# Optimization experiments

Hardware: AMD Instinct MI355X
Metric: run time of the kernel (lower is better)

## Reference

```python
import jax, jax.numpy as jnp
import numpy as np

NUM_CLASSES = 90
MAX_DET_POINTS = 5000
MAX_DET_PER_IMAGE = 100
IOU_THR = 0.5
NEG = -1e10
IMAGE_SIZE = 768


def _make_anchors(image_size=IMAGE_SIZE, min_level=3, num_levels=5, anchor_scale=4.0):
    """EfficientDet-style anchors, ordered (level, y, x, anchor-config), yxyx."""
    boxes_all = []
    for li in range(num_levels):
        stride = 2 ** (min_level + li)
        boxes_level = []
        for octave in range(3):
            for aspect in (1.0, 2.0, 0.5):
                base = anchor_scale * stride * 2.0 ** (octave / 3.0)
                ax = np.sqrt(aspect)
                half_x = base * ax / 2.0
                half_y = base / ax / 2.0
                x = np.arange(stride / 2.0, image_size, stride)
                y = np.arange(stride / 2.0, image_size, stride)
                xv, yv = np.meshgrid(x, y)  # [H, W], row-major matches NHWC flatten
                xv = xv.reshape(-1)
                yv = yv.reshape(-1)
                boxes = np.stack([yv - half_y, xv - half_x, yv + half_y, xv + half_x], axis=1)
                boxes_level.append(boxes[:, None, :])
        boxes_all.append(np.concatenate(boxes_level, axis=1).reshape(-1, 4))
    return np.concatenate(boxes_all, axis=0).astype(np.float32)


def setup_inputs() -> dict:
    key = jax.random.key(0)
    ks = jax.random.split(key, 10)
    B = 8
    hw = [96, 48, 24, 12, 6]
    inp = {}
    for i, s in enumerate(hw):
        inp[f"cls{i}"] = jax.random.normal(ks[i], (B, 810, s, s), jnp.float32)
        inp[f"box{i}"] = jax.random.normal(ks[5 + i], (B, 36, s, s), jnp.float32)
    inp["anchor_boxes"] = jnp.asarray(_make_anchors())
    return inp


def _decode_boxes(rel_codes, anchors):
    # anchors: yxyx; rel_codes: (ty, tx, th, tw) -> output xyxy
    ycenter_a = (anchors[..., 0] + anchors[..., 2]) / 2
    xcenter_a = (anchors[..., 1] + anchors[..., 3]) / 2
    ha = anchors[..., 2] - anchors[..., 0]
    wa = anchors[..., 3] - anchors[..., 1]
    ty, tx, th, tw = rel_codes[..., 0], rel_codes[..., 1], rel_codes[..., 2], rel_codes[..., 3]
    w = jnp.exp(tw) * wa
    h = jnp.exp(th) * ha
    yc = ty * ha + ycenter_a
    xc = tx * wa + xcenter_a
    return jnp.stack([xc - w / 2, yc - h / 2, xc + w / 2, yc + h / 2], axis=-1)


def _nms_indices(boxes, scores, classes, iou_thr=IOU_THR, max_out=MAX_DET_PER_IMAGE):
    """torchvision.batched_nms: class-offset boxes, greedy NMS, return idx + valid mask."""
    boxes = jax.lax.stop_gradient(boxes)
    scores = jax.lax.stop_gradient(scores)
    off = classes.astype(boxes.dtype) * (jnp.max(boxes) + 1.0)
    b = boxes + off[:, None]  # [N,4]
    area = (b[:, 2] - b[:, 0]) * (b[:, 3] - b[:, 1])

    def body(i, state):
        live, sel, val = state
        idx = jnp.argmax(live)
        ok = live[idx] > 0.0  # sigmoid scores are >0; suppressed are NEG
        bi = b[idx]
        ix = jnp.maximum(0.0, jnp.minimum(b[:, 2], bi[2]) - jnp.maximum(b[:, 0], bi[0]))
        iy = jnp.maximum(0.0, jnp.minimum(b[:, 3], bi[3]) - jnp.maximum(b[:, 1], bi[1]))
        inter = ix * iy
        iou = inter / (area + area[idx] - inter + 1e-8)
        live = jnp.where(iou > iou_thr, NEG, live).at[idx].set(NEG)
        return live, sel.at[i].set(idx), val.at[i].set(ok)

    state0 = (scores, jnp.zeros((max_out,), jnp.int32), jnp.zeros((max_out,), bool))
    _, sel, val = jax.lax.fori_loop(0, max_out, body, state0)
    return sel, val


def _forward(cls_levels, box_levels, anchor_boxes):
    B = cls_levels[0].shape[0]
    C = NUM_CLASSES
    # NCHW -> NHWC -> [B, A, C] / [B, A, 4], concat over levels
    cls_all = jnp.concatenate(
        [c.transpose(0, 2, 3, 1).reshape(B, -1, C) for c in cls_levels], axis=1)
    box_all = jnp.concatenate(
        [b.transpose(0, 2, 3, 1).reshape(B, -1, 4) for b in box_levels], axis=1)

    top_vals, top_idx = jax.lax.top_k(cls_all.reshape(B, -1), MAX_DET_POINTS)
    indices = top_idx // C  # anchor index
    classes = top_idx % C
    box_topk = jnp.take_along_axis(box_all, indices[..., None], axis=1)  # [B,K,4]
    anchors_sel = anchor_boxes[indices]  # [B,K,4]

    boxes = _decode_boxes(box_topk, anchors_sel)  # xyxy [B,K,4]
    scores = jax.nn.sigmoid(top_vals)  # [B,K]

    def per_image(bx, sc, cl):
        sel, val = _nms_indices(bx, sc, cl)
        det = jnp.concatenate(
            [bx[sel], sc[sel, None], (cl[sel] + 1).astype(bx.dtype)[:, None]], axis=1)
        return jnp.where(val[:, None], det, 0.0)  # pad invalid rows with zeros

    return jax.vmap(per_image)(boxes, scores, classes)  # [B, 100, 6]


def reference(cls0, cls1, cls2, cls3, cls4, box0, box1, box2, box3, box4, anchor_boxes):
    return _forward((cls0, cls1, cls2, cls3, cls4), (box0, box1, box2, box3, box4), anchor_boxes)
```

## Files before the change

kernel.cpp:

```cpp
#include <hip/hip_runtime.h>
#include <stdint.h>

#define KDET 5000
#define MAX_OUT 100
#define PRE_THR 2.5f
#define CAND_CAP 98304u
#define SEL_N 8192u
#define TOTAL_F 9943560u
#define STAGE_CAP 1024u
#define HBINS 2048u
#define FB 0x18040u
#define SEL_STRIDE 5120u

#define WS_CNT   0
#define WS_HIST  4096
#define WS_PMAX  69632
#define WS_CAND  131072
#define WS_SELG  6422528
#define WS_BX    6750208
#define WS_SC    7390208
#define WS_CL    7550208

__device__ __forceinline__ unsigned f2key(float f) {
  unsigned u = __float_as_uint(f);
  return u ^ (unsigned)(((int)u >> 31) | 0x80000000);
}

__global__ __launch_bounds__(256, 8) void scan_kernel(
    const float* __restrict__ c0, const float* __restrict__ c1,
    const float* __restrict__ c2, const float* __restrict__ c3,
    const float* __restrict__ c4,
    unsigned long long* __restrict__ cand,
    unsigned* __restrict__ cnt, unsigned* __restrict__ hist)
{
  __shared__ unsigned sh_hist[HBINS];
  __shared__ unsigned long long sh_cand[STAGE_CAP];
  __shared__ unsigned sh_ccnt;
  __shared__ unsigned sh_base;

  const unsigned img = blockIdx.y;
  const unsigned tid = threadIdx.x;
  const float* ptrs[5] = {c0, c1, c2, c3, c4};
  const unsigned lvlElems[5] = {7464960u, 1866240u, 466560u, 116640u, 29160u};
  const unsigned hw2s[5] = {9216u, 2304u, 576u, 144u, 36u};
  const unsigned fbases[5] = {0u, 7464960u, 9331200u, 9797760u, 9914400u};
  unsigned long long* candI = cand + (size_t)img * CAND_CAP;
  unsigned* histI = hist + img * HBINS;

  for (unsigned b = tid; b < HBINS; b += 256u) sh_hist[b] = 0u;
  if (tid == 0) sh_ccnt = 0u;
  __syncthreads();

#pragma unroll
  for (int lev = 0; lev < 5; ++lev) {
    const float4* p = (const float4*)(ptrs[lev] + (size_t)img * lvlElems[lev]);
    const unsigned n4 = lvlElems[lev] >> 2;
    const unsigned hw2 = hw2s[lev];
    const unsigned fbase = fbases[lev];
    const unsigned chunk = 256u * 4u;
    const unsigned sweep = gridDim.x * chunk;
    for (unsigned s0 = blockIdx.x * chunk; s0 < n4; s0 += sweep) {
      float4 v[4]; unsigned idxs[4]; bool ok[4];
#pragma unroll
      for (int u = 0; u < 4; ++u) {
        idxs[u] = s0 + (unsigned)u * 256u + tid;
        ok[u] = idxs[u] < n4;
        if (ok[u]) v[u] = p[idxs[u]];
      }
#pragma unroll
      for (int u = 0; u < 4; ++u) {
        if (!ok[u]) continue;
        float vs[4] = {v[u].x, v[u].y, v[u].z, v[u].w};
#pragma unroll
        for (int j = 0; j < 4; ++j) {
          float f = vs[j];
          if (f > PRE_THR) {
            unsigned key = f2key(f);
            unsigned bin = (key >> 15) - FB;
            if (bin > HBINS - 1u) bin = HBINS - 1u;
            atomicAdd(&sh_hist[bin], 1u);
            unsigned linear = idxs[u] * 4u + (unsigned)j;
            unsigned ch = linear / hw2;
            unsigned pos = linear - ch * hw2;
            unsigned F = fbase + pos * 810u + ch;
            unsigned slot = atomicAdd(&sh_ccnt, 1u);
            if (slot < STAGE_CAP)
              sh_cand[slot] = ((unsigned long long)key << 32) | (unsigned)(~F);
          }
        }
      }
    }
  }
  __syncthreads();

  unsigned n = sh_ccnt < STAGE_CAP ? sh_ccnt : STAGE_CAP;
  if (tid == 0) sh_base = atomicAdd(&cnt[img], n);
  __syncthreads();
  unsigned base = sh_base;
  for (unsigned k = tid; k < n; k += 256u) {
    unsigned slot = base + k;
    if (slot < CAND_CAP) candI[slot] = sh_cand[k];
  }
  for (unsigned b = tid; b < HBINS; b += 256u) {
    unsigned v = sh_hist[b];
    if (v) atomicAdd(&histI[b], v);
  }
}

__device__ __forceinline__ void bitonic_ce(unsigned long long* sb,
                                           unsigned i, unsigned ixj, bool desc) {
  unsigned long long a = sb[i], b = sb[ixj];
  if ((a < b) == desc) { sb[i] = b; sb[ixj] = a; }
}

__global__ __launch_bounds__(1024) void sort_kernel(
    const unsigned long long* __restrict__ cand, const unsigned* __restrict__ cnt,
    const unsigned* __restrict__ hist, unsigned long long* __restrict__ selG)
{
  const unsigned img = blockIdx.x;
  const unsigned tid = threadIdx.x;
  const unsigned wid = tid >> 6, lane = tid & 63u;
  __shared__ unsigned long long sb[SEL_N];
  __shared__ unsigned wsum[16];
  __shared__ unsigned sh_keyLow;
  __shared__ unsigned sh_scnt;

  const unsigned* histI = hist + img * HBINS;
  unsigned b0 = 2047u - 2u * tid;
  unsigned b1 = b0 - 1u;
  unsigned h0 = histI[b0], h1 = histI[b1];
  unsigned s = h0 + h1;
  unsigned inc = s;
#pragma unroll
  for (int off = 1; off < 64; off <<= 1) {
    unsigned nv = __shfl_up(inc, off, 64);
    if ((int)lane >= off) inc += nv;
  }
  if (lane == 63u) wsum[wid] = inc;
  if (tid == 0) { sh_keyLow = 0u; sh_scnt = 0u; }
  __syncthreads();
  if (tid < 64u) {
    unsigned v = (tid < 16u) ? wsum[tid] : 0u;
#pragma unroll
    for (int off = 1; off < 16; off <<= 1) {
      unsigned nv = __shfl_up(v, off, 64);
      if ((int)tid >= off) v += nv;
    }
    if (tid < 16u) wsum[tid] = v;
  }
  __syncthreads();
  unsigned excl = inc - s + (wid ? wsum[wid - 1] : 0u);
  if (excl < (unsigned)KDET && excl + s >= (unsigned)KDET) {
    unsigned binr = (excl + h0 >= (unsigned)KDET) ? b0 : b1;
    sh_keyLow = (binr + FB) << 15;
  }
  __syncthreads();
  const unsigned keyLow = sh_keyLow;

  unsigned M = cnt[img]; if (M > CAND_CAP) M = CAND_CAP;
  const unsigned long long* candI = cand + (size_t)img * CAND_CAP;
  for (unsigned i = tid; i < M; i += 1024u) {
    unsigned long long c = candI[i];
    if ((unsigned)(c >> 32) >= keyLow) {
      unsigned p = atomicAdd(&sh_scnt, 1u);
      if (p < SEL_N) sb[p] = c;
    }
  }
  __syncthreads();
  unsigned scnt = sh_scnt; if (scnt > SEL_N) scnt = SEL_N;
  for (unsigned i = scnt + tid; i < SEL_N; i += 1024u) sb[i] = 0ull;
  __syncthreads();

  for (unsigned k = 2; k <= SEL_N; k <<= 1) {
    for (unsigned j = k >> 1; j > 0; j >>= 1) {
      if (j >= 512u) {
        for (unsigned i = tid; i < SEL_N; i += 1024u) {
          unsigned ixj = i ^ j;
          if (ixj > i) bitonic_ce(sb, i, ixj, (i & k) == 0);
        }
        __syncthreads();
      } else {
        const unsigned base = wid * 512u;
#pragma unroll
        for (unsigned m = 0; m < 8; ++m) {
          unsigned i = base + m * 64u + lane;
          unsigned ixj = i ^ j;
          if (ixj > i) bitonic_ce(sb, i, ixj, (i & k) == 0);
        }
        asm volatile("" ::: "memory");
      }
    }
    __syncthreads();
  }

  unsigned long long* selI = selG + (size_t)img * SEL_STRIDE;
  for (unsigned i = tid; i < (unsigned)KDET; i += 1024u) selI[i] = sb[i];
}

__global__ __launch_bounds__(256) void decode_kernel(
    const float* __restrict__ x0, const float* __restrict__ x1,
    const float* __restrict__ x2, const float* __restrict__ x3,
    const float* __restrict__ x4, const float* __restrict__ anchors,
    const unsigned long long* __restrict__ selG,
    float* __restrict__ bx, float* __restrict__ sc, unsigned* __restrict__ cl,
    float* __restrict__ pmax)
{
  const unsigned img = blockIdx.y;
  const unsigned blk = blockIdx.x;
  const unsigned tid = threadIdx.x;
  __shared__ float wmax[4];
  const unsigned long long* selI = selG + (size_t)img * SEL_STRIDE;
  float* bxI = bx + (size_t)img * KDET * 4;
  float* scI = sc + (size_t)img * KDET;
  unsigned* clI = cl + (size_t)img * KDET;
  const unsigned start = blk * 625u;
  const unsigned end = start + 625u;

  float lmax = -3.4e38f;
  for (unsigned e = start + tid; e < end; e += 256u) {
    unsigned long long ent = selI[e];
    unsigned keyS = (unsigned)(ent >> 32);
    unsigned F = ~(unsigned)ent;
    if (F >= TOTAL_F) F = 0u;
    unsigned ubits = (keyS & 0x80000000u) ? (keyS ^ 0x80000000u) : ~keyS;
    float logit = __uint_as_float(ubits);
    unsigned anchor = F / 90u;
    unsigned clv = F - anchor * 90u;
    const float* bp; unsigned W, ab;
    if (anchor < 82944u)       { bp = x0; W = 96; ab = 0u; }
    else if (anchor < 103680u) { bp = x1; W = 48; ab = 82944u; }
    else if (anchor < 108864u) { bp = x2; W = 24; ab = 103680u; }
    else if (anchor < 110160u) { bp = x3; W = 12; ab = 108864u; }
    else                       { bp = x4; W = 6;  ab = 110160u; }
    unsigned rel = anchor - ab;
    unsigned cell = rel / 9u;
    unsigned a = rel - cell * 9u;
    unsigned y = cell / W;
    unsigned xx = cell - y * W;
    unsigned hw2 = W * W;
    size_t baseoff = ((size_t)img * 36u + a * 4u) * hw2 + (size_t)y * W + xx;
    float ty = bp[baseoff];
    float tx = bp[baseoff + hw2];
    float th = bp[baseoff + 2 * (size_t)hw2];
    float tw = bp[baseoff + 3 * (size_t)hw2];
    float A0 = anchors[anchor * 4u + 0], A1 = anchors[anchor * 4u + 1];
    float A2 = anchors[anchor * 4u + 2], A3 = anchors[anchor * 4u + 3];
    float yca = (A0 + A2) * 0.5f;
    float xca = (A1 + A3) * 0.5f;
    float ha = A2 - A0, wa = A3 - A1;
    float w = expf(tw) * wa;
    float h = expf(th) * ha;
    float yc = ty * ha + yca;
    float xc = tx * wa + xca;
    float X1 = xc - w * 0.5f, Y1 = yc - h * 0.5f;
    float X2 = xc + w * 0.5f, Y2 = yc + h * 0.5f;
    bxI[e * 4 + 0] = X1; bxI[e * 4 + 1] = Y1; bxI[e * 4 + 2] = X2; bxI[e * 4 + 3] = Y2;
    scI[e] = 1.0f / (1.0f + expf(-logit));
    clI[e] = clv;
    lmax = fmaxf(lmax, fmaxf(fmaxf(X1, Y1), fmaxf(X2, Y2)));
  }
#pragma unroll
  for (int off = 32; off > 0; off >>= 1)
    lmax = fmaxf(lmax, __shfl_down(lmax, off, 64));
  if ((tid & 63u) == 0) wmax[tid >> 6] = lmax;
  __syncthreads();
  if (tid == 0) {
    float m = fmaxf(fmaxf(wmax[0], wmax[1]), fmaxf(wmax[2], wmax[3]));
    pmax[img * 8u + blk] = m;
  }
}

__global__ __launch_bounds__(1024) void nms_kernel(
    const float* __restrict__ bx, const float* __restrict__ sc,
    const unsigned* __restrict__ cl, const float* __restrict__ pmax,
    float* __restrict__ out)
{
  const unsigned img = blockIdx.x;
  const unsigned tid = threadIdx.x;
  __shared__ float bo[KDET][4];
  __shared__ float ar[KDET];
  __shared__ float sh_gmax;
  __shared__ float kb0[MAX_OUT], kb1[MAX_OUT], kb2[MAX_OUT], kb3[MAX_OUT], karea[MAX_OUT];
  __shared__ int sh_kidx[MAX_OUT];
  __shared__ int sh_kept;

  if (tid < 64u) {
    float v = (tid < 8u) ? pmax[img * 8u + tid] : -3.4e38f;
#pragma unroll
    for (int off = 4; off > 0; off >>= 1)
      v = fmaxf(v, __shfl_down(v, off, 64));
    if (tid == 0) sh_gmax = v;
  }
  __syncthreads();
  const float gmax1 = sh_gmax + 1.0f;

  const float4* bx4 = (const float4*)(bx + (size_t)img * KDET * 4);
  const float* bxI = bx + (size_t)img * KDET * 4;
  const float* scI = sc + (size_t)img * KDET;
  const unsigned* clI = cl + (size_t)img * KDET;
  for (unsigned i = tid; i < (unsigned)KDET; i += 1024u) {
    float4 b = bx4[i];
    float offv = (float)clI[i] * gmax1;
    float X1 = b.x + offv, Y1 = b.y + offv, X2 = b.z + offv, Y2 = b.w + offv;
    bo[i][0] = X1; bo[i][1] = Y1; bo[i][2] = X2; bo[i][3] = Y2;
    ar[i] = (X2 - X1) * (Y2 - Y1);
  }
  __syncthreads();

  if (tid < 64u) {
    const int lane = (int)tid;
    int kept = 0;
    for (int jj = 0; jj < KDET && kept < MAX_OUT; ++jj) {
      float bjx1 = bo[jj][0], bjy1 = bo[jj][1];
      float bjx2 = bo[jj][2], bjy2 = bo[jj][3];
      float aj = ar[jj];
      int sup = 0;
      for (int m = lane; m < kept; m += 64) {
        float ix = fmaxf(0.0f, fminf(kb2[m], bjx2) - fmaxf(kb0[m], bjx1));
        float iy = fmaxf(0.0f, fminf(kb3[m], bjy2) - fmaxf(kb1[m], bjy1));
        float inter = ix * iy;
        float iou = inter / ((aj + karea[m]) - inter + 1e-8f);
        if (iou > 0.5f) sup = 1;
      }
      if (__any(sup)) continue;
      if (lane == 0) {
        kb0[kept] = bjx1; kb1[kept] = bjy1; kb2[kept] = bjx2; kb3[kept] = bjy2;
        karea[kept] = aj;
        sh_kidx[kept] = jj;
      }
      kept++;
    }
    if (lane == 0) sh_kept = kept;
  }
  __syncthreads();

  {
    const int kept = sh_kept;
    float* o = out + (size_t)img * 600;
    for (unsigned idx = tid; idx < 600u; idx += 1024u) {
      unsigned row = idx / 6u, col = idx - row * 6u;
      float v = 0.0f;
      if (row < (unsigned)kept) {
        int jj = sh_kidx[row];
        if (col < 4u)      v = bxI[jj * 4 + col];
        else if (col == 4) v = scI[jj];
        else               v = (float)(clI[jj] + 1u);
      }
      o[idx] = v;
    }
  }
}

extern "C" void kernel_launch(void* const* d_in, const int* in_sizes, int n_in,
                              void* d_out, int out_size, void* d_ws, size_t ws_size,
                              hipStream_t stream) {
  const int clsSz[5] = {59719680, 14929920, 3732480, 933120, 233280};
  const int boxSz[5] = {2654208, 663552, 165888, 41472, 10368};
  const float* cls[5] = {nullptr, nullptr, nullptr, nullptr, nullptr};
  const float* box[5] = {nullptr, nullptr, nullptr, nullptr, nullptr};
  const float* anchors = nullptr;
  for (int i = 0; i < n_in; ++i) {
    int s = in_sizes[i];
    for (int l = 0; l < 5; ++l) {
      if (s == clsSz[l]) cls[l] = (const float*)d_in[i];
      if (s == boxSz[l]) box[l] = (const float*)d_in[i];
    }
    if (s == 441936) anchors = (const float*)d_in[i];
  }
  if (!cls[0] || !box[0] || !anchors) {
    for (int l = 0; l < 5; ++l) { cls[l] = (const float*)d_in[2 * l]; box[l] = (const float*)d_in[2 * l + 1]; }
    anchors = (const float*)d_in[10];
  }

  char* ws = (char*)d_ws;
  unsigned* cnt = (unsigned*)(ws + WS_CNT);
  unsigned* hist = (unsigned*)(ws + WS_HIST);
  float* pmaxA = (float*)(ws + WS_PMAX);
  unsigned long long* cand = (unsigned long long*)(ws + WS_CAND);
  unsigned long long* selG = (unsigned long long*)(ws + WS_SELG);
  float* bxA = (float*)(ws + WS_BX);
  float* scA = (float*)(ws + WS_SC);
  unsigned* clA = (unsigned*)(ws + WS_CL);

  (void)hipMemsetAsync(ws, 0, WS_PMAX, stream);
  scan_kernel<<<dim3(256, 8), 256, 0, stream>>>(
      cls[0], cls[1], cls[2], cls[3], cls[4], cand, cnt, hist);
  sort_kernel<<<8, 1024, 0, stream>>>(cand, cnt, hist, selG);
  decode_kernel<<<dim3(8, 8), 256, 0, stream>>>(
      box[0], box[1], box[2], box[3], box[4], anchors, selG, bxA, scA, clA, pmaxA);
  nms_kernel<<<8, 1024, 0, stream>>>(bxA, scA, clA, pmaxA, (float*)d_out);
}
```

Before: 570.4 us.

## Fuse sort, decode and NMS into one kernel with bucketed lazy chunk sorting

Merges the sort, decode and NMS kernels into one per-image kernel. Candidates are scattered into histogram-bin buckets with per-bin atomic offsets, so the full 8192-element bitonic sort over all candidates goes away. Only small chunks are sorted as NMS reaches them, which allows early exit once 100 boxes are kept. The global-max class offset now needs an extra decode pass over all top-K entries. A fallback to the full sort handles oversized bins, and the design adds complexity around chunk boundaries and tie ordering.

After: 596.7 us. 1.05x slower.

```diff
diff --git a/kernel.cpp b/kernel.cpp
--- a/kernel.cpp
+++ b/kernel.cpp
@@ -10,16 +10,13 @@
 #define STAGE_CAP 1024u
 #define HBINS 2048u
 #define FB 0x18040u
-#define SEL_STRIDE 5120u
+#define CHUNKW 512u
+#define SC_CAP 1024u
 
 #define WS_CNT   0
 #define WS_HIST  4096
-#define WS_PMAX  69632
+#define WS_ZERO  69632
 #define WS_CAND  131072
-#define WS_SELG  6422528
-#define WS_BX    6750208
-#define WS_SC    7390208
-#define WS_CL    7550208
 
 __device__ __forceinline__ unsigned f2key(float f) {
   unsigned u = __float_as_uint(f);
@@ -113,18 +110,114 @@
   if ((a < b) == desc) { sb[i] = b; sb[ixj] = a; }
 }
 
-__global__ __launch_bounds__(1024) void sort_kernel(
-    const unsigned long long* __restrict__ cand, const unsigned* __restrict__ cnt,
-    const unsigned* __restrict__ hist, unsigned long long* __restrict__ selG)
+__device__ __forceinline__ unsigned npow2(unsigned n) {
+  unsigned m = 1u;
+  while (m < n) m <<= 1u;
+  return m;
+}
+
+__device__ void bitonic_desc(unsigned long long* a, unsigned m,
+                             unsigned tid, unsigned wid, unsigned lane) {
+  for (unsigned k = 2; k <= m; k <<= 1) {
+    for (unsigned j = k >> 1; j; j >>= 1) {
+      if (j >= 512u) {
+        for (unsigned i = tid; i < m; i += 1024u) {
+          unsigned ixj = i ^ j;
+          if (ixj > i) bitonic_ce(a, i, ixj, (i & k) == 0);
+        }
+        __syncthreads();
+      } else {
+        unsigned base = wid * 512u;
+        if (base < m) {
+          unsigned lim = m - base;
+#pragma unroll
+          for (unsigned t = 0; t < 8; ++t) {
+            unsigned io = t * 64u + lane;
+            if (io < lim) {
+              unsigned i = base + io;
+              unsigned ixj = i ^ j;
+              if (ixj > i) bitonic_ce(a, i, ixj, (i & k) == 0);
+            }
+          }
+        }
+        asm volatile("" ::: "memory");
+      }
+    }
+    __syncthreads();
+  }
+}
+
+__device__ __forceinline__ void decode_entry(
+    unsigned long long ent, unsigned img,
+    const float* __restrict__ x0, const float* __restrict__ x1,
+    const float* __restrict__ x2, const float* __restrict__ x3,
+    const float* __restrict__ x4, const float* __restrict__ anchors,
+    float b4[4])
+{
+  unsigned F = ~(unsigned)ent;
+  if (F >= TOTAL_F) F = 0u;
+  unsigned anchor = F / 90u;
+  const float* bp; unsigned W, ab;
+  if (anchor < 82944u)       { bp = x0; W = 96; ab = 0u; }
+  else if (anchor < 103680u) { bp = x1; W = 48; ab = 82944u; }
+  else if (anchor < 108864u) { bp = x2; W = 24; ab = 103680u; }
+  else if (anchor < 110160u) { bp = x3; W = 12; ab = 108864u; }
+  else                       { bp = x4; W = 6;  ab = 110160u; }
+  unsigned rel = anchor - ab;
+  unsigned cell = rel / 9u;
+  unsigned a = rel - cell * 9u;
+  unsigned y = cell / W;
+  unsigned xx = cell - y * W;
+  unsigned hw2 = W * W;
+  size_t baseoff = ((size_t)img * 36u + a * 4u) * hw2 + (size_t)y * W + xx;
+  float ty = bp[baseoff];
+  float tx = bp[baseoff + hw2];
+  float th = bp[baseoff + 2 * (size_t)hw2];
+  float tw = bp[baseoff + 3 * (size_t)hw2];
+  float A0 = anchors[anchor * 4u + 0], A1 = anchors[anchor * 4u + 1];
+  float A2 = anchors[anchor * 4u + 2], A3 = anchors[anchor * 4u + 3];
+  float yca = (A0 + A2) * 0.5f;
+  float xca = (A1 + A3) * 0.5f;
+  float ha = A2 - A0, wa = A3 - A1;
+  float w = expf(tw) * wa;
+  float h = expf(th) * ha;
+  float yc = ty * ha + yca;
+  float xc = tx * wa + xca;
+  b4[0] = xc - w * 0.5f; b4[1] = yc - h * 0.5f;
+  b4[2] = xc + w * 0.5f; b4[3] = yc + h * 0.5f;
+}
+
+__global__ __launch_bounds__(1024) void select_nms_kernel(
+    const float* __restrict__ x0, const float* __restrict__ x1,
+    const float* __restrict__ x2, const float* __restrict__ x3,
+    const float* __restrict__ x4, const float* __restrict__ anchors,
+    const unsigned long long* __restrict__ cand,
+    const unsigned* __restrict__ cnt, const unsigned* __restrict__ hist,
+    float* __restrict__ out)
 {
   const unsigned img = blockIdx.x;
   const unsigned tid = threadIdx.x;
   const unsigned wid = tid >> 6, lane = tid & 63u;
+
   __shared__ unsigned long long sb[SEL_N];
+  __shared__ unsigned long long sc8[SC_CAP];
+  __shared__ float bo[SC_CAP][4];
+  __shared__ unsigned bofs[HBINS];
+  __shared__ unsigned sh_bound[16];
   __shared__ unsigned wsum[16];
-  __shared__ unsigned sh_keyLow;
-  __shared__ unsigned sh_scnt;
-
+  __shared__ float fred[16];
+  __shared__ unsigned sh_keyLow, sh_binLow, sh_SabA, sh_cntA;
+  __shared__ unsigned sh_Sab0, sh_cnt0;
+  __shared__ int sh_flags;
+  __shared__ unsigned sh_p1;
+  __shared__ float sh_gmax;
+  __shared__ float kb0[MAX_OUT], kb1[MAX_OUT], kb2[MAX_OUT], kb3[MAX_OUT];
+  __shared__ float karea[MAX_OUT];
+  __shared__ float kout[MAX_OUT][6];
+  __shared__ int sh_kept;
+
+  if (tid == 0) { sh_keyLow = 0u; sh_binLow = 0u; sh_flags = 0; sh_kept = 0; }
+  if (tid < 16u) sh_bound[tid] = 0u;
   const unsigned* histI = hist + img * HBINS;
   unsigned b0 = 2047u - 2u * tid;
   unsigned b1 = b0 - 1u;
@@ -137,7 +230,6 @@
     if ((int)lane >= off) inc += nv;
   }
   if (lane == 63u) wsum[wid] = inc;
-  if (tid == 0) { sh_keyLow = 0u; sh_scnt = 0u; }
   __syncthreads();
   if (tid < 64u) {
     unsigned v = (tid < 16u) ? wsum[tid] : 0u;
@@ -150,204 +242,185 @@
   }
   __syncthreads();
   unsigned excl = inc - s + (wid ? wsum[wid - 1] : 0u);
+  bofs[b0] = excl;
+  bofs[b1] = excl + h0;
   if (excl < (unsigned)KDET && excl + s >= (unsigned)KDET) {
-    unsigned binr = (excl + h0 >= (unsigned)KDET) ? b0 : b1;
+    bool first = (excl + h0 >= (unsigned)KDET);
+    unsigned binr = first ? b0 : b1;
     sh_keyLow = (binr + FB) << 15;
-  }
-  __syncthreads();
+    sh_binLow = binr;
+    sh_SabA = first ? excl : excl + h0;
+    sh_cntA = first ? h0 : h1;
+  }
+  if (tid == 1023u) { sh_Sab0 = excl + h0; sh_cnt0 = h1; }
+  __syncthreads();
+
   const unsigned keyLow = sh_keyLow;
+  unsigned binLow, Sabove, cntLow;
+  if (keyLow) { binLow = sh_binLow; Sabove = sh_SabA; cntLow = sh_cntA; }
+  else        { binLow = 0u;        Sabove = sh_Sab0; cntLow = sh_cnt0; }
+  const unsigned selCount = Sabove + cntLow;
+
+  {
+    unsigned e0 = excl + h0;
+    unsigned e1 = e0 + h1;
+    if (b0 > binLow && h0 != 0u) {
+      if (h0 > CHUNKW) sh_flags = 1;
+      unsigned e = e0 > SEL_N ? SEL_N : e0;
+      atomicMax(&sh_bound[(e - 1u) / CHUNKW], e);
+    }
+    if (b1 > binLow && h1 != 0u) {
+      if (h1 > CHUNKW) sh_flags = 1;
+      unsigned e = e1 > SEL_N ? SEL_N : e1;
+      atomicMax(&sh_bound[(e - 1u) / CHUNKW], e);
+    }
+    if (b0 == binLow && h0 > SC_CAP) sh_flags = 1;
+    if (b1 == binLow && h1 > SC_CAP) sh_flags = 1;
+  }
+  __syncthreads();
+
+  const unsigned selCap = selCount < SEL_N ? selCount : SEL_N;
+  const unsigned NT = selCap < (unsigned)KDET ? selCap : (unsigned)KDET;
+  const int fullSort = sh_flags;
 
   unsigned M = cnt[img]; if (M > CAND_CAP) M = CAND_CAP;
   const unsigned long long* candI = cand + (size_t)img * CAND_CAP;
   for (unsigned i = tid; i < M; i += 1024u) {
     unsigned long long c = candI[i];
-    if ((unsigned)(c >> 32) >= keyLow) {
-      unsigned p = atomicAdd(&sh_scnt, 1u);
-      if (p < SEL_N) sb[p] = c;
-    }
-  }
-  __syncthreads();
-  unsigned scnt = sh_scnt; if (scnt > SEL_N) scnt = SEL_N;
-  for (unsigned i = scnt + tid; i < SEL_N; i += 1024u) sb[i] = 0ull;
-  __syncthreads();
-
-  for (unsigned k = 2; k <= SEL_N; k <<= 1) {
-    for (unsigned j = k >> 1; j > 0; j >>= 1) {
-      if (j >= 512u) {
-        for (unsigned i = tid; i < SEL_N; i += 1024u) {
-          unsigned ixj = i ^ j;
-          if (ixj > i) bitonic_ce(sb, i, ixj, (i & k) == 0);
-        }
-        __syncthreads();
-      } else {
-        const unsigned base = wid * 512u;
-#pragma unroll
-        for (unsigned m = 0; m < 8; ++m) {
-          unsigned i = base + m * 64u + lane;
-          unsigned ixj = i ^ j;
-          if (ixj > i) bitonic_ce(sb, i, ixj, (i & k) == 0);
-        }
-        asm volatile("" ::: "memory");
-      }
-    }
-    __syncthreads();
-  }
-
-  unsigned long long* selI = selG + (size_t)img * SEL_STRIDE;
-  for (unsigned i = tid; i < (unsigned)KDET; i += 1024u) selI[i] = sb[i];
-}
-
-__global__ __launch_bounds__(256) void decode_kernel(
-    const float* __restrict__ x0, const float* __restrict__ x1,
-    const float* __restrict__ x2, const float* __restrict__ x3,
-    const float* __restrict__ x4, const float* __restrict__ anchors,
-    const unsigned long long* __restrict__ selG,
-    float* __restrict__ bx, float* __restrict__ sc, unsigned* __restrict__ cl,
-    float* __restrict__ pmax)
-{
-  const unsigned img = blockIdx.y;
-  const unsigned blk = blockIdx.x;
-  const unsigned tid = threadIdx.x;
-  __shared__ float wmax[4];
-  const unsigned long long* selI = selG + (size_t)img * SEL_STRIDE;
-  float* bxI = bx + (size_t)img * KDET * 4;
-  float* scI = sc + (size_t)img * KDET;
-  unsigned* clI = cl + (size_t)img * KDET;
-  const unsigned start = blk * 625u;
-  const unsigned end = start + 625u;
+    unsigned key = (unsigned)(c >> 32);
+    if (key >= keyLow) {
+      unsigned bin = (key >> 15) - FB;
+      if (bin > HBINS - 1u) bin = HBINS - 1u;
+      unsigned pos = atomicAdd(&bofs[bin], 1u);
+      if (pos < SEL_N) sb[pos] = c;
+    }
+  }
+  __syncthreads();
+
+  if (fullSort) {
+    for (unsigned i = selCap + tid; i < SEL_N; i += 1024u) sb[i] = 0ull;
+    __syncthreads();
+    bitonic_desc(sb, SEL_N, tid, wid, lane);
+  } else if (cntLow > 1u) {
+    unsigned segEnd = Sabove + cntLow; if (segEnd > SEL_N) segEnd = SEL_N;
+    unsigned n = segEnd - Sabove;
+    if (n > 1u) {
+      unsigned m = npow2(n);
+      for (unsigned i = tid; i < m; i += 1024u)
+        sc8[i] = (i < n) ? sb[Sabove + i] : 0ull;
+      __syncthreads();
+      bitonic_desc(sc8, m, tid, wid, lane);
+      for (unsigned i = tid; i < n; i += 1024u) sb[Sabove + i] = sc8[i];
+      __syncthreads();
+    }
+  }
 
   float lmax = -3.4e38f;
-  for (unsigned e = start + tid; e < end; e += 256u) {
-    unsigned long long ent = selI[e];
-    unsigned keyS = (unsigned)(ent >> 32);
-    unsigned F = ~(unsigned)ent;
-    if (F >= TOTAL_F) F = 0u;
-    unsigned ubits = (keyS & 0x80000000u) ? (keyS ^ 0x80000000u) : ~keyS;
-    float logit = __uint_as_float(ubits);
-    unsigned anchor = F / 90u;
-    unsigned clv = F - anchor * 90u;
-    const float* bp; unsigned W, ab;
-    if (anchor < 82944u)       { bp = x0; W = 96; ab = 0u; }
-    else if (anchor < 103680u) { bp = x1; W = 48; ab = 82944u; }
-    else if (anchor < 108864u) { bp = x2; W = 24; ab = 103680u; }
-    else if (anchor < 110160u) { bp = x3; W = 12; ab = 108864u; }
-    else                       { bp = x4; W = 6;  ab = 110160u; }
-    unsigned rel = anchor - ab;
-    unsigned cell = rel / 9u;
-    unsigned a = rel - cell * 9u;
-    unsigned y = cell / W;
-    unsigned xx = cell - y * W;
-    unsigned hw2 = W * W;
-    size_t baseoff = ((size_t)img * 36u + a * 4u) * hw2 + (size_t)y * W + xx;
-    float ty = bp[baseoff];
-    float tx = bp[baseoff + hw2];
-    float th = bp[baseoff + 2 * (size_t)hw2];
-    float tw = bp[baseoff + 3 * (size_t)hw2];
-    float A0 = anchors[anchor * 4u + 0], A1 = anchors[anchor * 4u + 1];
-    float A2 = anchors[anchor * 4u + 2], A3 = anchors[anchor * 4u + 3];
-    float yca = (A0 + A2) * 0.5f;
-    float xca = (A1 + A3) * 0.5f;
-    float ha = A2 - A0, wa = A3 - A1;
-    float w = expf(tw) * wa;
-    float h = expf(th) * ha;
-    float yc = ty * ha + yca;
-    float xc = tx * wa + xca;
-    float X1 = xc - w * 0.5f, Y1 = yc - h * 0.5f;
-    float X2 = xc + w * 0.5f, Y2 = yc + h * 0.5f;
-    bxI[e * 4 + 0] = X1; bxI[e * 4 + 1] = Y1; bxI[e * 4 + 2] = X2; bxI[e * 4 + 3] = Y2;
-    scI[e] = 1.0f / (1.0f + expf(-logit));
-    clI[e] = clv;
-    lmax = fmaxf(lmax, fmaxf(fmaxf(X1, Y1), fmaxf(X2, Y2)));
+  for (unsigned e = tid; e < NT; e += 1024u) {
+    float b4[4];
+    decode_entry(sb[e], img, x0, x1, x2, x3, x4, anchors, b4);
+    lmax = fmaxf(lmax, fmaxf(fmaxf(b4[0], b4[1]), fmaxf(b4[2], b4[3])));
   }
 #pragma unroll
   for (int off = 32; off > 0; off >>= 1)
     lmax = fmaxf(lmax, __shfl_down(lmax, off, 64));
-  if ((tid & 63u) == 0) wmax[tid >> 6] = lmax;
-  __syncthreads();
-  if (tid == 0) {
-    float m = fmaxf(fmaxf(wmax[0], wmax[1]), fmaxf(wmax[2], wmax[3]));
-    pmax[img * 8u + blk] = m;
-  }
-}
-
-__global__ __launch_bounds__(1024) void nms_kernel(
-    const float* __restrict__ bx, const float* __restrict__ sc,
-    const unsigned* __restrict__ cl, const float* __restrict__ pmax,
-    float* __restrict__ out)
-{
-  const unsigned img = blockIdx.x;
-  const unsigned tid = threadIdx.x;
-  __shared__ float bo[KDET][4];
-  __shared__ float ar[KDET];
-  __shared__ float sh_gmax;
-  __shared__ float kb0[MAX_OUT], kb1[MAX_OUT], kb2[MAX_OUT], kb3[MAX_OUT], karea[MAX_OUT];
-  __shared__ int sh_kidx[MAX_OUT];
-  __shared__ int sh_kept;
-
-  if (tid < 64u) {
-    float v = (tid < 8u) ? pmax[img * 8u + tid] : -3.4e38f;
-#pragma unroll
-    for (int off = 4; off > 0; off >>= 1)
-      v = fmaxf(v, __shfl_down(v, off, 64));
-    if (tid == 0) sh_gmax = v;
+  if (lane == 0u) fred[wid] = lmax;
+  __syncthreads();
+  if (tid == 0u) {
+    float g = fred[0];
+#pragma unroll
+    for (int i2 = 1; i2 < 16; ++i2) g = fmaxf(g, fred[i2]);
+    sh_gmax = g;
   }
   __syncthreads();
   const float gmax1 = sh_gmax + 1.0f;
 
-  const float4* bx4 = (const float4*)(bx + (size_t)img * KDET * 4);
-  const float* bxI = bx + (size_t)img * KDET * 4;
-  const float* scI = sc + (size_t)img * KDET;
-  const unsigned* clI = cl + (size_t)img * KDET;
-  for (unsigned i = tid; i < (unsigned)KDET; i += 1024u) {
-    float4 b = bx4[i];
-    float offv = (float)clI[i] * gmax1;
-    float X1 = b.x + offv, Y1 = b.y + offv, X2 = b.z + offv, Y2 = b.w + offv;
-    bo[i][0] = X1; bo[i][1] = Y1; bo[i][2] = X2; bo[i][3] = Y2;
-    ar[i] = (X2 - X1) * (Y2 - Y1);
-  }
-  __syncthreads();
-
-  if (tid < 64u) {
-    const int lane = (int)tid;
-    int kept = 0;
-    for (int jj = 0; jj < KDET && kept < MAX_OUT; ++jj) {
-      float bjx1 = bo[jj][0], bjy1 = bo[jj][1];
-      float bjx2 = bo[jj][2], bjy2 = bo[jj][3];
-      float aj = ar[jj];
-      int sup = 0;
-      for (int m = lane; m < kept; m += 64) {
-        float ix = fmaxf(0.0f, fminf(kb2[m], bjx2) - fmaxf(kb0[m], bjx1));
-        float iy = fmaxf(0.0f, fminf(kb3[m], bjy2) - fmaxf(kb1[m], bjy1));
-        float inter = ix * iy;
-        float iou = inter / ((aj + karea[m]) - inter + 1e-8f);
-        if (iou > 0.5f) sup = 1;
+  unsigned processed = 0u;
+  while (true) {
+    if (processed >= NT || sh_kept >= MAX_OUT) break;
+    if (tid == 0u) {
+      unsigned p0v = processed, p1;
+      if (fullSort) {
+        p1 = p0v + CHUNKW; if (p1 > NT) p1 = NT;
+      } else if (p0v < Sabove) {
+        unsigned c0 = p0v / CHUNKW;
+        unsigned bA = sh_bound[c0];
+        unsigned bB = sh_bound[c0 + 1u];
+        p1 = 0u;
+        if (bA > p0v) p1 = bA;
+        if (bB > p0v && bB > p1) p1 = bB;
+        if (p1 == 0u) { p1 = p0v + CHUNKW; if (p1 > NT) p1 = NT; }
+      } else {
+        unsigned segEnd = Sabove + cntLow;
+        if (segEnd > NT) segEnd = NT;
+        p1 = p0v + CHUNKW; if (p1 > segEnd) p1 = segEnd;
       }
-      if (__any(sup)) continue;
-      if (lane == 0) {
-        kb0[kept] = bjx1; kb1[kept] = bjy1; kb2[kept] = bjx2; kb3[kept] = bjy2;
-        karea[kept] = aj;
-        sh_kidx[kept] = jj;
+      if (p1 <= p0v) p1 = (NT < p0v + CHUNKW) ? NT : p0v + CHUNKW;
+      if (p1 > p0v + SC_CAP) p1 = p0v + SC_CAP;
+      sh_p1 = p1;
+    }
+    __syncthreads();
+    const unsigned p0 = processed, p1 = sh_p1;
+    const unsigned n = p1 - p0;
+
+    unsigned m = npow2(n);
+    for (unsigned i = tid; i < m; i += 1024u)
+      sc8[i] = (i < n) ? sb[p0 + i] : 0ull;
+    __syncthreads();
+    if (n > 1u) bitonic_desc(sc8, m, tid, wid, lane);
+
+    for (unsigned e = tid; e < n; e += 1024u) {
+      float b4[4];
+      decode_entry(sc8[e], img, x0, x1, x2, x3, x4, anchors, b4);
+      bo[e][0] = b4[0]; bo[e][1] = b4[1]; bo[e][2] = b4[2]; bo[e][3] = b4[3];
+    }
+    __syncthreads();
+
+    if (tid < 64u) {
+      int kept = sh_kept;
+      for (unsigned jj = 0; jj < n && kept < MAX_OUT; ++jj) {
+        unsigned long long ent = sc8[jj];
+        unsigned keyS = (unsigned)(ent >> 32);
+        unsigned F = ~(unsigned)ent; if (F >= TOTAL_F) F = 0u;
+        unsigned anchor = F / 90u;
+        unsigned clv = F - anchor * 90u;
+        float offv = (float)clv * gmax1;
+        float rx1 = bo[jj][0], ry1 = bo[jj][1], rx2 = bo[jj][2], ry2 = bo[jj][3];
+        float X1 = rx1 + offv, Y1 = ry1 + offv;
+        float X2 = rx2 + offv, Y2 = ry2 + offv;
+        float aj = (X2 - X1) * (Y2 - Y1);
+        int sup = 0;
+        for (int mI = (int)lane; mI < kept; mI += 64) {
+          float ix = fmaxf(0.0f, fminf(kb2[mI], X2) - fmaxf(kb0[mI], X1));
+          float iy = fmaxf(0.0f, fminf(kb3[mI], Y2) - fmaxf(kb1[mI], Y1));
+          float inter = ix * iy;
+          float iou = inter / ((aj + karea[mI]) - inter + 1e-8f);
+          if (iou > 0.5f) sup = 1;
+        }
+        if (__any(sup)) continue;
+        if (lane == 0u) {
+          kb0[kept] = X1; kb1[kept] = Y1; kb2[kept] = X2; kb3[kept] = Y2;
+          karea[kept] = aj;
+          unsigned ubits = (keyS & 0x80000000u) ? (keyS ^ 0x80000000u) : ~keyS;
+          float logit = __uint_as_float(ubits);
+          kout[kept][0] = rx1; kout[kept][1] = ry1;
+          kout[kept][2] = rx2; kout[kept][3] = ry2;
+          kout[kept][4] = 1.0f / (1.0f + expf(-logit));
+          kout[kept][5] = (float)(clv + 1u);
+        }
+        kept++;
       }
-      kept++;
-    }
-    if (lane == 0) sh_kept = kept;
-  }
-  __syncthreads();
-
-  {
-    const int kept = sh_kept;
-    float* o = out + (size_t)img * 600;
-    for (unsigned idx = tid; idx < 600u; idx += 1024u) {
-      unsigned row = idx / 6u, col = idx - row * 6u;
-      float v = 0.0f;
-      if (row < (unsigned)kept) {
-        int jj = sh_kidx[row];
-        if (col < 4u)      v = bxI[jj * 4 + col];
-        else if (col == 4) v = scI[jj];
-        else               v = (float)(clI[jj] + 1u);
-      }
-      o[idx] = v;
-    }
+      if (tid == 0u) sh_kept = kept;
+    }
+    processed = p1;
+    __syncthreads();
+  }
+
+  const int keptF = sh_kept;
+  float* o = out + (size_t)img * 600u;
+  for (unsigned idx = tid; idx < 600u; idx += 1024u) {
+    unsigned row = idx / 6u, col = idx - row * 6u;
+    o[idx] = (row < (unsigned)keptF) ? kout[row][col] : 0.0f;
   }
 }
 
@@ -375,18 +448,12 @@
   char* ws = (char*)d_ws;
   unsigned* cnt = (unsigned*)(ws + WS_CNT);
   unsigned* hist = (unsigned*)(ws + WS_HIST);
-  float* pmaxA = (float*)(ws + WS_PMAX);
   unsigned long long* cand = (unsigned long long*)(ws + WS_CAND);
-  unsigned long long* selG = (unsigned long long*)(ws + WS_SELG);
-  float* bxA = (float*)(ws + WS_BX);
-  float* scA = (float*)(ws + WS_SC);
-  unsigned* clA = (unsigned*)(ws + WS_CL);
-
-  (void)hipMemsetAsync(ws, 0, WS_PMAX, stream);
+
+  (void)hipMemsetAsync(ws, 0, WS_ZERO, stream);
   scan_kernel<<<dim3(256, 8), 256, 0, stream>>>(
       cls[0], cls[1], cls[2], cls[3], cls[4], cand, cnt, hist);
-  sort_kernel<<<8, 1024, 0, stream>>>(cand, cnt, hist, selG);
-  decode_kernel<<<dim3(8, 8), 256, 0, stream>>>(
-      box[0], box[1], box[2], box[3], box[4], anchors, selG, bxA, scA, clA, pmaxA);
-  nms_kernel<<<8, 1024, 0, stream>>>(bxA, scA, clA, pmaxA, (float*)d_out);
-}
+  select_nms_kernel<<<8, 1024, 0, stream>>>(
+      box[0], box[1], box[2], box[3], box[4], anchors, cand, cnt, hist,
+      (float*)d_out);
+}
```

## Replace full bitonic sort with histogram bucket scatter and partial segment sorts

Applied to the files above, without the earlier changes.

Instead of sorting all 8192 candidates with a full bitonic network, the select kernel scatters candidates into histogram-bin order using the prefix offsets. It then sorts only the boundary bin segment and a short prefix of chunks. The unsorted tail beyond the sorted prefix is sorted lazily in the NMS kernel, and only when fewer than 100 boxes have been kept by that point. This cuts the per-image sort work at the cost of more complex control flow, extra shared memory in the NMS kernel, and a fallback full sort when the bins are too large.

Result: faster. 541.3 us (-5.1%).

```diff
diff --git a/kernel.cpp b/kernel.cpp
--- a/kernel.cpp
+++ b/kernel.cpp
@@ -10,16 +10,21 @@
 #define STAGE_CAP 1024u
 #define HBINS 2048u
 #define FB 0x18040u
+#define CHUNKW 512u
+#define SC2_CAP 2048u
+#define NMSK_CAP 4096u
 #define SEL_STRIDE 5120u
 
 #define WS_CNT   0
 #define WS_HIST  4096
-#define WS_PMAX  69632
-#define WS_CAND  131072
-#define WS_SELG  6422528
-#define WS_BX    6750208
-#define WS_SC    7390208
-#define WS_CL    7550208
+#define WS_ZERO  69632
+#define WS_META  69632
+#define WS_PMAX  69760
+#define WS_SELG  131072
+#define WS_BX    458752
+#define WS_SC    1098752
+#define WS_CL    1258752
+#define WS_CAND  1441792
 
 __device__ __forceinline__ unsigned f2key(float f) {
   unsigned u = __float_as_uint(f);
@@ -113,17 +118,104 @@
   if ((a < b) == desc) { sb[i] = b; sb[ixj] = a; }
 }
 
-__global__ __launch_bounds__(1024) void sort_kernel(
+__device__ __forceinline__ unsigned npow2(unsigned n) {
+  unsigned m = 1u;
+  while (m < n) m <<= 1u;
+  return m;
+}
+
+__device__ void bitonic_desc(unsigned long long* a, unsigned m,
+                             unsigned tid, unsigned wid, unsigned lane) {
+  for (unsigned k = 2; k <= m; k <<= 1) {
+    for (unsigned j = k >> 1; j; j >>= 1) {
+      if (j >= 512u) {
+        for (unsigned i = tid; i < m; i += 1024u) {
+          unsigned ixj = i ^ j;
+          if (ixj > i) bitonic_ce(a, i, ixj, (i & k) == 0);
+        }
+        __syncthreads();
+      } else {
+        unsigned base = wid * 512u;
+        if (base < m) {
+          unsigned lim = m - base; if (lim > 512u) lim = 512u;
+#pragma unroll
+          for (unsigned t = 0; t < 8; ++t) {
+            unsigned io = t * 64u + lane;
+            if (io < lim) {
+              unsigned i = base + io;
+              unsigned ixj = i ^ j;
+              if (ixj > i) bitonic_ce(a, i, ixj, (i & k) == 0);
+            }
+          }
+        }
+        asm volatile("" ::: "memory");
+      }
+    }
+    __syncthreads();
+  }
+}
+
+__device__ __forceinline__ void bitonic_ce_pair(unsigned long long* kk,
+                                                unsigned short* pp,
+                                                unsigned i, unsigned ixj, bool desc) {
+  unsigned long long a = kk[i], b = kk[ixj];
+  if ((a < b) == desc) {
+    kk[i] = b; kk[ixj] = a;
+    unsigned short t = pp[i]; pp[i] = pp[ixj]; pp[ixj] = t;
+  }
+}
+
+__device__ void bitonic_desc_pair(unsigned long long* kk, unsigned short* pp,
+                                  unsigned m, unsigned tid, unsigned wid,
+                                  unsigned lane) {
+  for (unsigned k = 2; k <= m; k <<= 1) {
+    for (unsigned j = k >> 1; j; j >>= 1) {
+      if (j >= 512u) {
+        for (unsigned i = tid; i < m; i += 1024u) {
+          unsigned ixj = i ^ j;
+          if (ixj > i) bitonic_ce_pair(kk, pp, i, ixj, (i & k) == 0);
+        }
+        __syncthreads();
+      } else {
+        unsigned base = wid * 512u;
+        if (base < m) {
+          unsigned lim = m - base; if (lim > 512u) lim = 512u;
+#pragma unroll
+          for (unsigned t = 0; t < 8; ++t) {
+            unsigned io = t * 64u + lane;
+            if (io < lim) {
+              unsigned i = base + io;
+              unsigned ixj = i ^ j;
+              if (ixj > i) bitonic_ce_pair(kk, pp, i, ixj, (i & k) == 0);
+            }
+          }
+        }
+        asm volatile("" ::: "memory");
+      }
+    }
+    __syncthreads();
+  }
+}
+
+__global__ __launch_bounds__(1024) void select_kernel(
     const unsigned long long* __restrict__ cand, const unsigned* __restrict__ cnt,
-    const unsigned* __restrict__ hist, unsigned long long* __restrict__ selG)
+    const unsigned* __restrict__ hist, unsigned long long* __restrict__ selG,
+    unsigned* __restrict__ meta)
 {
   const unsigned img = blockIdx.x;
   const unsigned tid = threadIdx.x;
   const unsigned wid = tid >> 6, lane = tid & 63u;
   __shared__ unsigned long long sb[SEL_N];
+  __shared__ unsigned long long sc2[SC2_CAP];
+  __shared__ unsigned bofs[HBINS];
+  __shared__ unsigned sh_bound[16];
   __shared__ unsigned wsum[16];
-  __shared__ unsigned sh_keyLow;
-  __shared__ unsigned sh_scnt;
+  __shared__ unsigned sh_keyLow, sh_binLow, sh_SabA, sh_cntA, sh_Sab0, sh_cnt0;
+  __shared__ int sh_flags;
+
+  if (tid == 0) { sh_keyLow = 0u; sh_binLow = 0u; sh_flags = 0; }
+  if (tid < 16u) sh_bound[tid] = 0u;
+  for (unsigned i = tid; i < SEL_N; i += 1024u) sb[i] = 0ull;
 
   const unsigned* histI = hist + img * HBINS;
   unsigned b0 = 2047u - 2u * tid;
@@ -137,7 +229,6 @@
     if ((int)lane >= off) inc += nv;
   }
   if (lane == 63u) wsum[wid] = inc;
-  if (tid == 0) { sh_keyLow = 0u; sh_scnt = 0u; }
   __syncthreads();
   if (tid < 64u) {
     unsigned v = (tid < 16u) ? wsum[tid] : 0u;
@@ -150,51 +241,114 @@
   }
   __syncthreads();
   unsigned excl = inc - s + (wid ? wsum[wid - 1] : 0u);
+  bofs[b0] = excl;
+  bofs[b1] = excl + h0;
   if (excl < (unsigned)KDET && excl + s >= (unsigned)KDET) {
-    unsigned binr = (excl + h0 >= (unsigned)KDET) ? b0 : b1;
+    bool first = (excl + h0 >= (unsigned)KDET);
+    unsigned binr = first ? b0 : b1;
     sh_keyLow = (binr + FB) << 15;
-  }
-  __syncthreads();
+    sh_binLow = binr;
+    sh_SabA = first ? excl : excl + h0;
+    sh_cntA = first ? h0 : h1;
+  }
+  if (tid == 1023u) { sh_Sab0 = excl + h0; sh_cnt0 = h1; }
+  __syncthreads();
+
   const unsigned keyLow = sh_keyLow;
+  unsigned binLow, Sabove, cntLow;
+  if (keyLow) { binLow = sh_binLow; Sabove = sh_SabA; cntLow = sh_cntA; }
+  else        { binLow = 0u;        Sabove = sh_Sab0; cntLow = sh_cnt0; }
+  const unsigned selCount = Sabove + cntLow;
+  const unsigned NT = selCount < (unsigned)KDET ? selCount : (unsigned)KDET;
+
+  {
+    unsigned e0 = excl + h0;
+    unsigned e1 = e0 + h1;
+    if (b0 > binLow && h0 != 0u) {
+      if (h0 > CHUNKW) sh_flags = 1;
+      unsigned e = e0 > SEL_N ? SEL_N : e0;
+      atomicMax(&sh_bound[(e - 1u) / CHUNKW], e);
+    }
+    if (b1 > binLow && h1 != 0u) {
+      if (h1 > CHUNKW) sh_flags = 1;
+      unsigned e = e1 > SEL_N ? SEL_N : e1;
+      atomicMax(&sh_bound[(e - 1u) / CHUNKW], e);
+    }
+    if (b0 == binLow && h0 > SC2_CAP) sh_flags = 1;
+    if (b1 == binLow && h1 > SC2_CAP) sh_flags = 1;
+  }
+  __syncthreads();
+
+  unsigned prefEnd = sh_bound[0];
+  if (sh_bound[1] > prefEnd) prefEnd = sh_bound[1];
+  if (sh_bound[2] > prefEnd) prefEnd = sh_bound[2];
+  if (sh_bound[3] > prefEnd) prefEnd = sh_bound[3];
+  int doFull = sh_flags;
+  unsigned sortedEnd;
+  if (!doFull) {
+    if (Sabove <= prefEnd) sortedEnd = (unsigned)KDET;
+    else {
+      sortedEnd = prefEnd;
+      if ((unsigned)KDET - sortedEnd > NMSK_CAP) doFull = 1;
+    }
+  }
+  if (doFull) sortedEnd = (unsigned)KDET;
 
   unsigned M = cnt[img]; if (M > CAND_CAP) M = CAND_CAP;
   const unsigned long long* candI = cand + (size_t)img * CAND_CAP;
-  for (unsigned i = tid; i < M; i += 1024u) {
-    unsigned long long c = candI[i];
-    if ((unsigned)(c >> 32) >= keyLow) {
-      unsigned p = atomicAdd(&sh_scnt, 1u);
-      if (p < SEL_N) sb[p] = c;
-    }
-  }
-  __syncthreads();
-  unsigned scnt = sh_scnt; if (scnt > SEL_N) scnt = SEL_N;
-  for (unsigned i = scnt + tid; i < SEL_N; i += 1024u) sb[i] = 0ull;
-  __syncthreads();
-
-  for (unsigned k = 2; k <= SEL_N; k <<= 1) {
-    for (unsigned j = k >> 1; j > 0; j >>= 1) {
-      if (j >= 512u) {
-        for (unsigned i = tid; i < SEL_N; i += 1024u) {
-          unsigned ixj = i ^ j;
-          if (ixj > i) bitonic_ce(sb, i, ixj, (i & k) == 0);
-        }
+  for (unsigned i = tid; i < M; i += 4096u) {
+    unsigned long long c[4]; bool ok[4];
+#pragma unroll
+    for (int u = 0; u < 4; ++u) {
+      unsigned ii = i + (unsigned)u * 1024u;
+      ok[u] = ii < M;
+      c[u] = ok[u] ? candI[ii] : 0ull;
+    }
+#pragma unroll
+    for (int u = 0; u < 4; ++u) {
+      if (!ok[u]) continue;
+      unsigned key = (unsigned)(c[u] >> 32);
+      if (key >= keyLow) {
+        unsigned bin = (key >> 15) - FB;
+        if (bin > HBINS - 1u) bin = HBINS - 1u;
+        unsigned pos = atomicAdd(&bofs[bin], 1u);
+        if (pos < SEL_N) sb[pos] = c[u];
+      }
+    }
+  }
+  __syncthreads();
+
+  if (doFull) {
+    bitonic_desc(sb, SEL_N, tid, wid, lane);
+  } else {
+    if (cntLow > 1u) {
+      unsigned segEnd = Sabove + cntLow; if (segEnd > SEL_N) segEnd = SEL_N;
+      unsigned n = segEnd - Sabove;
+      if (n > 1u) {
+        unsigned m = npow2(n);
+        for (unsigned i = tid; i < m; i += 1024u)
+          sc2[i] = (i < n) ? sb[Sabove + i] : 0ull;
         __syncthreads();
-      } else {
-        const unsigned base = wid * 512u;
-#pragma unroll
-        for (unsigned m = 0; m < 8; ++m) {
-          unsigned i = base + m * 64u + lane;
-          unsigned ixj = i ^ j;
-          if (ixj > i) bitonic_ce(sb, i, ixj, (i & k) == 0);
-        }
-        asm volatile("" ::: "memory");
-      }
-    }
-    __syncthreads();
+        bitonic_desc(sc2, m, tid, wid, lane);
+        for (unsigned i = tid; i < n; i += 1024u) sb[Sabove + i] = sc2[i];
+        __syncthreads();
+      }
+    }
+    if (prefEnd > 1u) {
+      unsigned n = prefEnd;
+      unsigned m = npow2(n);
+      for (unsigned i = tid; i < m; i += 1024u)
+        sc2[i] = (i < n) ? sb[i] : 0ull;
+      __syncthreads();
+      bitonic_desc(sc2, m, tid, wid, lane);
+      for (unsigned i = tid; i < n; i += 1024u) sb[i] = sc2[i];
+      __syncthreads();
+    }
   }
 
   unsigned long long* selI = selG + (size_t)img * SEL_STRIDE;
   for (unsigned i = tid; i < (unsigned)KDET; i += 1024u) selI[i] = sb[i];
+  if (tid == 0) meta[img] = sortedEnd;
 }
 
 __global__ __launch_bounds__(256) void decode_kernel(
@@ -273,12 +427,17 @@
 __global__ __launch_bounds__(1024) void nms_kernel(
     const float* __restrict__ bx, const float* __restrict__ sc,
     const unsigned* __restrict__ cl, const float* __restrict__ pmax,
+    const unsigned long long* __restrict__ selG,
+    const unsigned* __restrict__ meta,
     float* __restrict__ out)
 {
   const unsigned img = blockIdx.x;
   const unsigned tid = threadIdx.x;
+  const unsigned wid = tid >> 6, lane = tid & 63u;
   __shared__ float bo[KDET][4];
   __shared__ float ar[KDET];
+  __shared__ unsigned long long kk[NMSK_CAP];
+  __shared__ unsigned short pp[NMSK_CAP];
   __shared__ float sh_gmax;
   __shared__ float kb0[MAX_OUT], kb1[MAX_OUT], kb2[MAX_OUT], kb3[MAX_OUT], karea[MAX_OUT];
   __shared__ int sh_kidx[MAX_OUT];
@@ -293,6 +452,7 @@
   }
   __syncthreads();
   const float gmax1 = sh_gmax + 1.0f;
+  const unsigned sortedEnd = meta[img];
 
   const float4* bx4 = (const float4*)(bx + (size_t)img * KDET * 4);
   const float* bxI = bx + (size_t)img * KDET * 4;
@@ -307,32 +467,56 @@
   }
   __syncthreads();
 
+#define NMS_STEP(ROW, KEPT) do { \
+    unsigned row_ = (ROW); \
+    float bjx1 = bo[row_][0], bjy1 = bo[row_][1]; \
+    float bjx2 = bo[row_][2], bjy2 = bo[row_][3]; \
+    float aj = ar[row_]; \
+    int sup = 0; \
+    for (int mI = (int)lane; mI < (KEPT); mI += 64) { \
+      float ix = fmaxf(0.0f, fminf(kb2[mI], bjx2) - fmaxf(kb0[mI], bjx1)); \
+      float iy = fmaxf(0.0f, fminf(kb3[mI], bjy2) - fmaxf(kb1[mI], bjy1)); \
+      float inter = ix * iy; \
+      float iou = inter / ((aj + karea[mI]) - inter + 1e-8f); \
+      if (iou > 0.5f) sup = 1; \
+    } \
+    if (!__any(sup)) { \
+      if (lane == 0) { \
+        kb0[KEPT] = bjx1; kb1[KEPT] = bjy1; kb2[KEPT] = bjx2; kb3[KEPT] = bjy2; \
+        karea[KEPT] = aj; sh_kidx[KEPT] = (int)row_; \
+      } \
+      (KEPT)++; \
+    } \
+  } while (0)
+
   if (tid < 64u) {
-    const int lane = (int)tid;
     int kept = 0;
-    for (int jj = 0; jj < KDET && kept < MAX_OUT; ++jj) {
-      float bjx1 = bo[jj][0], bjy1 = bo[jj][1];
-      float bjx2 = bo[jj][2], bjy2 = bo[jj][3];
-      float aj = ar[jj];
-      int sup = 0;
-      for (int m = lane; m < kept; m += 64) {
-        float ix = fmaxf(0.0f, fminf(kb2[m], bjx2) - fmaxf(kb0[m], bjx1));
-        float iy = fmaxf(0.0f, fminf(kb3[m], bjy2) - fmaxf(kb1[m], bjy1));
-        float inter = ix * iy;
-        float iou = inter / ((aj + karea[m]) - inter + 1e-8f);
-        if (iou > 0.5f) sup = 1;
-      }
-      if (__any(sup)) continue;
-      if (lane == 0) {
-        kb0[kept] = bjx1; kb1[kept] = bjy1; kb2[kept] = bjx2; kb3[kept] = bjy2;
-        karea[kept] = aj;
-        sh_kidx[kept] = jj;
-      }
-      kept++;
-    }
+    for (unsigned jj = 0; jj < sortedEnd && kept < MAX_OUT; ++jj)
+      NMS_STEP(jj, kept);
     if (lane == 0) sh_kept = kept;
   }
   __syncthreads();
+
+  if (sh_kept < MAX_OUT && sortedEnd < (unsigned)KDET) {
+    const unsigned rem = (unsigned)KDET - sortedEnd;
+    const unsigned m = npow2(rem);
+    const unsigned long long* selI = selG + (size_t)img * SEL_STRIDE;
+    for (unsigned i = tid; i < m; i += 1024u) {
+      if (i < rem) { kk[i] = selI[sortedEnd + i]; pp[i] = (unsigned short)i; }
+      else         { kk[i] = 0ull; pp[i] = 0; }
+    }
+    __syncthreads();
+    bitonic_desc_pair(kk, pp, m, tid, wid, lane);
+    if (tid < 64u) {
+      int kept = sh_kept;
+      for (unsigned j = 0; j < rem && kept < MAX_OUT; ++j)
+        NMS_STEP(sortedEnd + (unsigned)pp[j], kept);
+      if (lane == 0) sh_kept = kept;
+    }
+    __syncthreads();
+  }
+
+#undef NMS_STEP
 
   {
     const int kept = sh_kept;
@@ -375,18 +559,20 @@
   char* ws = (char*)d_ws;
   unsigned* cnt = (unsigned*)(ws + WS_CNT);
   unsigned* hist = (unsigned*)(ws + WS_HIST);
+  unsigned* metaA = (unsigned*)(ws + WS_META);
   float* pmaxA = (float*)(ws + WS_PMAX);
-  unsigned long long* cand = (unsigned long long*)(ws + WS_CAND);
   unsigned long long* selG = (unsigned long long*)(ws + WS_SELG);
   float* bxA = (float*)(ws + WS_BX);
   float* scA = (float*)(ws + WS_SC);
   unsigned* clA = (unsigned*)(ws + WS_CL);
-
-  (void)hipMemsetAsync(ws, 0, WS_PMAX, stream);
+  unsigned long long* cand = (unsigned long long*)(ws + WS_CAND);
+
+  (void)hipMemsetAsync(ws, 0, WS_ZERO, stream);
   scan_kernel<<<dim3(256, 8), 256, 0, stream>>>(
       cls[0], cls[1], cls[2], cls[3], cls[4], cand, cnt, hist);
-  sort_kernel<<<8, 1024, 0, stream>>>(cand, cnt, hist, selG);
+  select_kernel<<<8, 1024, 0, stream>>>(cand, cnt, hist, selG, metaA);
   decode_kernel<<<dim3(8, 8), 256, 0, stream>>>(
       box[0], box[1], box[2], box[3], box[4], anchors, selG, bxA, scA, clA, pmaxA);
-  nms_kernel<<<8, 1024, 0, stream>>>(bxA, scA, clA, pmaxA, (float*)d_out);
-}
+  nms_kernel<<<8, 1024, 0, stream>>>(bxA, scA, clA, pmaxA, selG, metaA,
+                                     (float*)d_out);
+}
```
